# Optimization experiments

Measured on AMD Instinct MI355X. Metric: run time of the kernel, lower is better.

The kernel has to match this reference:

```python
import jax, jax.numpy as jnp
import numpy as np
import math

B, L, H, NH = 8, 200, 128, 2
HD = H // NH  # head dim = 64
TIME_VOCAB = 32
LN_EPS = 1e-12


def setup_inputs() -> dict:
    key = jax.random.key(0)
    ks = jax.random.split(key, 16)
    rn = lambda k, shape, s=0.02: (jax.random.normal(k, shape, jnp.float32) * s)
    return {
        "input_tensor": jax.random.normal(ks[0], (B, L, H), jnp.float32),
        "time_seq": jnp.sort(jax.random.randint(ks[1], (B, L), 0, 100000, jnp.int64), axis=-1),
        "attention_mask": jnp.zeros((B, 1, L, L), jnp.float32),
        "Wq": rn(ks[2], (H, H)), "bq": jnp.zeros((H,), jnp.float32),
        "Wk": rn(ks[3], (H, H)), "bk": jnp.zeros((H,), jnp.float32),
        "Wv": rn(ks[4], (H, H)), "bv": jnp.zeros((H,), jnp.float32),
        "Wd": rn(ks[5], (H, H)), "bd": jnp.zeros((H,), jnp.float32),
        "ln_g": jnp.ones((H,), jnp.float32), "ln_b": jnp.zeros((H,), jnp.float32),
        "key_time_table": rn(ks[6], (TIME_VOCAB, H)),
        "value_time_table": rn(ks[7], (TIME_VOCAB, H)),
        "key_pos_table": rn(ks[8], (L, H)),
        "value_pos_table": rn(ks[9], (L, H)),
    }


def _split_heads(x):
    # [B, L, H] -> [B, NH, L, HD]
    b, l, _ = x.shape
    return x.reshape(b, l, NH, HD).transpose(0, 2, 1, 3)


def reference(input_tensor, time_seq, attention_mask,
              Wq, bq, Wk, bk, Wv, bv, Wd, bd, ln_g, ln_b,
              key_time_table, value_time_table, key_pos_table, value_pos_table):
    b, l, h = input_tensor.shape

    # position embeddings (same for all batches)
    kpos = key_pos_table[:l].reshape(l, NH, HD).transpose(1, 0, 2)[None]    # [1,NH,L,HD]
    vpos = value_pos_table[:l].reshape(l, NH, HD).transpose(1, 0, 2)[None]  # [1,NH,L,HD]

    q = _split_heads(input_tensor @ Wq + bq)  # [B,NH,L,HD]
    k = _split_heads(input_tensor @ Wk + bk)
    v = _split_heads(input_tensor @ Wv + bv)

    scores = jnp.einsum('bhqd,bhkd->bhqk', q, k + kpos)

    # time decay: diff[b,i,j] = floor(log(1 + |t_i - t_j|))
    t = time_seq
    diff_idx = jnp.log1p(jnp.abs(t[:, :, None] - t[:, None, :]).astype(jnp.float32)).astype(jnp.int32)  # [B,L,L]

    # [B,L,L,H] -> [B,NH,L,L,HD]
    kt = key_time_table[diff_idx].reshape(b, l, l, NH, HD).transpose(0, 3, 1, 2, 4)
    vt = value_time_table[diff_idx].reshape(b, l, l, NH, HD).transpose(0, 3, 1, 2, 4)

    time_scores = jnp.einsum('bhqd,bhqkd->bhqk', q, kt)

    scores = (scores + time_scores) / math.sqrt(HD)
    scores = scores + attention_mask  # additive mask, broadcast over heads

    probs = jax.nn.softmax(scores, axis=-1)  # attn_dropout is identity in eval

    ctx = jnp.einsum('bhqk,bhkd->bhqd', probs, v + vpos)
    # NOTE: original uses raw (masked, pre-softmax) attention_scores here
    time_ctx = jnp.einsum('bhqk,bhqkd->bhqd', scores, vt)
    ctx = ctx + time_ctx

    ctx = ctx.transpose(0, 2, 1, 3).reshape(b, l, h)  # merge heads
    hidden = ctx @ Wd + bd                            # out_dropout identity in eval

    x = hidden + input_tensor
    mu = x.mean(-1, keepdims=True)
    var = ((x - mu) ** 2).mean(-1, keepdims=True)
    return (x - mu) / jnp.sqrt(var + LN_EPS) * ln_g + ln_b
```

## Files before the change

kernel.cpp:

```cpp
#include <hip/hip_runtime.h>
#include <math.h>

#define B_ 8
#define L_ 200
#define H_ 128
#define NH_ 2
#define HD_ 64
#define LP_ 256
#define TV_ 32

__global__ void zero_kt_kernel(float* __restrict__ kt){
    kt[blockIdx.x * 256 + threadIdx.x] = 0.f;
}

__global__ __launch_bounds__(128)
void qkv_kernel(const float* __restrict__ X,
                const float* __restrict__ Wq, const float* __restrict__ bq,
                const float* __restrict__ Wk, const float* __restrict__ bk,
                const float* __restrict__ Wv, const float* __restrict__ bv,
                const float* __restrict__ kpt, const float* __restrict__ vpt,
                float* __restrict__ Q, float* __restrict__ Kt, float* __restrict__ Vp){
    const int row = blockIdx.x;
    const int m   = blockIdx.y;
    const int j   = threadIdx.x;
    const int b   = row / L_, l = row % L_;
    __shared__ float xs[H_];
    xs[j] = X[row * H_ + j];
    __syncthreads();
    const float* W = (m == 0) ? Wq : ((m == 1) ? Wk : Wv);
    float acc = 0.f;
    #pragma unroll 8
    for (int i = 0; i < H_; ++i) acc += xs[i] * W[i * H_ + j];
    const int h = j >> 6, d = j & 63;
    if (m == 0) {
        Q[row * H_ + j] = acc + bq[j];
    } else if (m == 1) {
        float v = acc + bk[j] + kpt[l * H_ + j];
        Kt[(((b * NH_ + h) * HD_) + d) * LP_ + l] = v;
    } else {
        float v = acc + bv[j] + vpt[l * H_ + j];
        Vp[(((b * NH_ + h) * L_) + l) * HD_ + d] = v;
    }
}

__global__ __launch_bounds__(256)
void attn_kernel(const float* __restrict__ Q, const float* __restrict__ Kt,
                 const float* __restrict__ Vp, const int* __restrict__ tseq,
                 const float* __restrict__ mask,
                 const float* __restrict__ ktt, const float* __restrict__ vtt,
                 float* __restrict__ ctx){
    const int wave = threadIdx.x >> 6, lane = threadIdx.x & 63;
    const int gq = blockIdx.x * 4 + wave;
    const int q  = gq % L_;
    const int bh = gq / L_;
    const int h  = bh % NH_, b = bh / NH_;

    __shared__ __align__(16) float qs [4][HD_];
    __shared__            float qkt[4][TV_];
    __shared__            float ss [4][TV_];
    __shared__ __align__(16) float ps [4][LP_];

    qs[wave][lane] = Q[(b * L_ + q) * H_ + h * HD_ + lane];
    if (lane < TV_) ss[wave][lane] = 0.f;
    __syncthreads();

    if (lane < TV_) {
        float a = 0.f;
        #pragma unroll 8
        for (int d = 0; d < HD_; ++d) a += qs[wave][d] * ktt[lane * H_ + h * HD_ + d];
        qkt[wave][lane] = a;
    }
    __syncthreads();

    const int tq = tseq[b * L_ + q];

    const float4* kt4 = (const float4*)(Kt + (size_t)bh * HD_ * LP_);
    float4 s4 = make_float4(0.f, 0.f, 0.f, 0.f);
    #pragma unroll 4
    for (int d = 0; d < HD_; ++d) {
        const float qd = qs[wave][d];
        const float4 kv = kt4[d * (LP_ / 4) + lane];
        s4.x += qd * kv.x; s4.y += qd * kv.y; s4.z += qd * kv.z; s4.w += qd * kv.w;
    }
    float sv[4] = {s4.x, s4.y, s4.z, s4.w};
    const int k0 = lane * 4;
    float mx = -INFINITY;
    #pragma unroll
    for (int jj = 0; jj < 4; ++jj) {
        const int k = k0 + jj;
        if (k < L_) {
            int dt = tq - tseq[b * L_ + k]; if (dt < 0) dt = -dt;
            int idx = (int)log1pf((float)dt);
            if (idx > TV_ - 1) idx = TV_ - 1;
            float s = (sv[jj] + qkt[wave][idx]) * 0.125f
                      + mask[((size_t)b * L_ + q) * L_ + k];
            sv[jj] = s;
            atomicAdd(&ss[wave][idx], s);
            if (s > mx) mx = s;
        } else sv[jj] = -INFINITY;
    }
    for (int off = 32; off; off >>= 1) { float o = __shfl_xor(mx, off); if (o > mx) mx = o; }
    float sum = 0.f, ev[4];
    #pragma unroll
    for (int jj = 0; jj < 4; ++jj) {
        float e = (k0 + jj < L_) ? __expf(sv[jj] - mx) : 0.f;
        ev[jj] = e; sum += e;
    }
    for (int off = 32; off; off >>= 1) sum += __shfl_xor(sum, off);
    ((float4*)ps[wave])[lane] = make_float4(ev[0], ev[1], ev[2], ev[3]);
    __syncthreads();

    const float inv = 1.f / sum;
    const float* vp = Vp + (size_t)bh * L_ * HD_;
    float c = 0.f;
    #pragma unroll 4
    for (int k = 0; k < L_; ++k) c += ps[wave][k] * vp[k * HD_ + lane];
    c *= inv;
    float tc = 0.f;
    #pragma unroll 8
    for (int i = 0; i < TV_; ++i) tc += ss[wave][i] * vtt[i * H_ + h * HD_ + lane];
    ctx[((size_t)b * L_ + q) * H_ + h * HD_ + lane] = c + tc;
}

__global__ __launch_bounds__(128)
void out_kernel(const float* __restrict__ ctx, const float* __restrict__ Wd,
                const float* __restrict__ bd, const float* __restrict__ X,
                const float* __restrict__ g, const float* __restrict__ bb,
                float* __restrict__ out){
    const int row = blockIdx.x, j = threadIdx.x;
    __shared__ float cs[H_];
    __shared__ float red[4];
    cs[j] = ctx[row * H_ + j];
    __syncthreads();
    float acc = 0.f;
    #pragma unroll 8
    for (int i = 0; i < H_; ++i) acc += cs[i] * Wd[i * H_ + j];
    const float x = acc + bd[j] + X[row * H_ + j];

    const int wave = j >> 6, lane = j & 63;
    float s = x;
    for (int off = 32; off; off >>= 1) s += __shfl_xor(s, off);
    if (lane == 0) red[wave] = s;
    __syncthreads();
    const float mean = (red[0] + red[1]) * (1.f / H_);
    const float dx = x - mean;
    float s2 = dx * dx;
    for (int off = 32; off; off >>= 1) s2 += __shfl_xor(s2, off);
    if (lane == 0) red[wave + 2] = s2;
    __syncthreads();
    const float var = (red[2] + red[3]) * (1.f / H_);
    const float y = dx * rsqrtf(var + 1e-12f) * g[j] + bb[j];
    out[row * H_ + j] = y;
}

extern "C" void kernel_launch(void* const* d_in, const int* in_sizes, int n_in,
                              void* d_out, int out_size, void* d_ws, size_t ws_size,
                              hipStream_t stream) {
    const float* X    = (const float*)d_in[0];
    const int*   tseq = (const int*)  d_in[1];
    const float* mask = (const float*)d_in[2];
    const float* Wq = (const float*)d_in[3],  *bq = (const float*)d_in[4];
    const float* Wk = (const float*)d_in[5],  *bk = (const float*)d_in[6];
    const float* Wv = (const float*)d_in[7],  *bv = (const float*)d_in[8];
    const float* Wd = (const float*)d_in[9],  *bd = (const float*)d_in[10];
    const float* g  = (const float*)d_in[11], *bb = (const float*)d_in[12];
    const float* ktt = (const float*)d_in[13], *vtt = (const float*)d_in[14];
    const float* kpt = (const float*)d_in[15], *vpt = (const float*)d_in[16];

    float* ws  = (float*)d_ws;
    float* Q   = ws;
    float* Kt  = Q   + B_ * L_ * H_;
    float* Vp  = Kt  + B_ * NH_ * HD_ * LP_;
    float* ctx = Vp  + B_ * L_ * H_;

    zero_kt_kernel<<<B_ * NH_ * HD_ * LP_ / 256, 256, 0, stream>>>(Kt);
    dim3 g1(B_ * L_, 3);
    qkv_kernel<<<g1, 128, 0, stream>>>(X, Wq, bq, Wk, bk, Wv, bv, kpt, vpt, Q, Kt, Vp);
    attn_kernel<<<B_ * NH_ * L_ / 4, 256, 0, stream>>>(Q, Kt, Vp, tseq, mask, ktt, vtt, ctx);
    out_kernel<<<B_ * L_, 128, 0, stream>>>(ctx, Wd, bd, X, g, bb, (float*)d_out);
}
```

Before: 141.5 us.

## Fuse attention with output projection and LayerNorm, batch QKV rows per block

Merges the attention kernel and the output-projection/LayerNorm kernel into one 512-thread kernel per batch and 4 queries, keeping ctx in shared memory instead of a global round trip. The QKV projection now computes 8 rows per block so each weight load is reused across rows. The Kt zeroing kernel is removed, and mask and time_seq reads are vectorised. Several __syncthreads are dropped on the basis that each wave only touches its own shared slices. Padded Kt columns are no longer zeroed and can hold stale data, but their scores are forced to -inf.

```diff
diff --git a/kernel.cpp b/kernel.cpp
--- a/kernel.cpp
+++ b/kernel.cpp
@@ -8,10 +8,8 @@
 #define HD_ 64
 #define LP_ 256
 #define TV_ 32
-
-__global__ void zero_kt_kernel(float* __restrict__ kt){
-    kt[blockIdx.x * 256 + threadIdx.x] = 0.f;
-}
+#define RQ_ 8
+#define TQ_ 4
 
 __global__ __launch_bounds__(128)
 void qkv_kernel(const float* __restrict__ X,
@@ -20,84 +18,104 @@
                 const float* __restrict__ Wv, const float* __restrict__ bv,
                 const float* __restrict__ kpt, const float* __restrict__ vpt,
                 float* __restrict__ Q, float* __restrict__ Kt, float* __restrict__ Vp){
-    const int row = blockIdx.x;
-    const int m   = blockIdx.y;
-    const int j   = threadIdx.x;
-    const int b   = row / L_, l = row % L_;
-    __shared__ float xs[H_];
-    xs[j] = X[row * H_ + j];
+    const int r0 = blockIdx.x * RQ_;
+    const int m  = blockIdx.y;
+    const int j  = threadIdx.x;
+    __shared__ float xs[RQ_][H_];
+    #pragma unroll
+    for (int r = 0; r < RQ_; ++r) xs[r][j] = X[(r0 + r) * H_ + j];
     __syncthreads();
     const float* W = (m == 0) ? Wq : ((m == 1) ? Wk : Wv);
-    float acc = 0.f;
-    #pragma unroll 8
-    for (int i = 0; i < H_; ++i) acc += xs[i] * W[i * H_ + j];
+    float acc[RQ_];
+    #pragma unroll
+    for (int r = 0; r < RQ_; ++r) acc[r] = 0.f;
+    #pragma unroll 4
+    for (int i = 0; i < H_; ++i) {
+        const float w = W[i * H_ + j];
+        #pragma unroll
+        for (int r = 0; r < RQ_; ++r) acc[r] += xs[r][i] * w;
+    }
     const int h = j >> 6, d = j & 63;
     if (m == 0) {
-        Q[row * H_ + j] = acc + bq[j];
+        const float bj = bq[j];
+        #pragma unroll
+        for (int r = 0; r < RQ_; ++r) Q[(r0 + r) * H_ + j] = acc[r] + bj;
     } else if (m == 1) {
-        float v = acc + bk[j] + kpt[l * H_ + j];
-        Kt[(((b * NH_ + h) * HD_) + d) * LP_ + l] = v;
+        const float bj = bk[j];
+        #pragma unroll
+        for (int r = 0; r < RQ_; ++r) {
+            const int row = r0 + r, b = row / L_, l = row % L_;
+            Kt[((b * NH_ + h) * HD_ + d) * LP_ + l] = acc[r] + bj + kpt[l * H_ + j];
+        }
     } else {
-        float v = acc + bv[j] + vpt[l * H_ + j];
-        Vp[(((b * NH_ + h) * L_) + l) * HD_ + d] = v;
+        const float bj = bv[j];
+        #pragma unroll
+        for (int r = 0; r < RQ_; ++r) {
+            const int row = r0 + r, b = row / L_, l = row % L_;
+            Vp[((b * NH_ + h) * L_ + l) * HD_ + d] = acc[r] + bj + vpt[l * H_ + j];
+        }
     }
 }
 
-__global__ __launch_bounds__(256)
-void attn_kernel(const float* __restrict__ Q, const float* __restrict__ Kt,
-                 const float* __restrict__ Vp, const int* __restrict__ tseq,
-                 const float* __restrict__ mask,
-                 const float* __restrict__ ktt, const float* __restrict__ vtt,
-                 float* __restrict__ ctx){
-    const int wave = threadIdx.x >> 6, lane = threadIdx.x & 63;
-    const int gq = blockIdx.x * 4 + wave;
-    const int q  = gq % L_;
-    const int bh = gq / L_;
-    const int h  = bh % NH_, b = bh / NH_;
+__global__ __launch_bounds__(512)
+void attn_out_kernel(const float* __restrict__ Q, const float* __restrict__ Kt,
+                     const float* __restrict__ Vp, const int* __restrict__ tseq,
+                     const float* __restrict__ mask,
+                     const float* __restrict__ ktt, const float* __restrict__ vtt,
+                     const float* __restrict__ Wd, const float* __restrict__ bd,
+                     const float* __restrict__ X, const float* __restrict__ g,
+                     const float* __restrict__ bb, float* __restrict__ out){
+    const int b  = blockIdx.x / (L_ / TQ_);
+    const int q0 = (blockIdx.x % (L_ / TQ_)) * TQ_;
+    const int w  = threadIdx.x >> 6, lane = threadIdx.x & 63;
+    const int h  = w & 1, qr = w >> 1, q = q0 + qr;
+    const int bh = b * NH_ + h;
 
-    __shared__ __align__(16) float qs [4][HD_];
-    __shared__            float qkt[4][TV_];
-    __shared__            float ss [4][TV_];
-    __shared__ __align__(16) float ps [4][LP_];
+    __shared__ __align__(16) float qs [8][HD_];
+    __shared__ float qkt[8][TV_];
+    __shared__ float ss [8][TV_];
+    __shared__ __align__(16) float ps [8][LP_];
+    __shared__ float ctx_s[TQ_][H_];
+    __shared__ float red1[8], red2[8];
 
-    qs[wave][lane] = Q[(b * L_ + q) * H_ + h * HD_ + lane];
-    if (lane < TV_) ss[wave][lane] = 0.f;
-    __syncthreads();
-
+    qs[w][lane] = Q[(b * L_ + q) * H_ + h * HD_ + lane];
+    if (lane < TV_) ss[w][lane] = 0.f;
     if (lane < TV_) {
         float a = 0.f;
         #pragma unroll 8
-        for (int d = 0; d < HD_; ++d) a += qs[wave][d] * ktt[lane * H_ + h * HD_ + d];
-        qkt[wave][lane] = a;
+        for (int d = 0; d < HD_; ++d) a += qs[w][d] * ktt[lane * H_ + h * HD_ + d];
+        qkt[w][lane] = a;
     }
-    __syncthreads();
-
-    const int tq = tseq[b * L_ + q];
 
     const float4* kt4 = (const float4*)(Kt + (size_t)bh * HD_ * LP_);
     float4 s4 = make_float4(0.f, 0.f, 0.f, 0.f);
     #pragma unroll 4
     for (int d = 0; d < HD_; ++d) {
-        const float qd = qs[wave][d];
+        const float qd = qs[w][d];
         const float4 kv = kt4[d * (LP_ / 4) + lane];
         s4.x += qd * kv.x; s4.y += qd * kv.y; s4.z += qd * kv.z; s4.w += qd * kv.w;
     }
     float sv[4] = {s4.x, s4.y, s4.z, s4.w};
     const int k0 = lane * 4;
     float mx = -INFINITY;
-    #pragma unroll
-    for (int jj = 0; jj < 4; ++jj) {
-        const int k = k0 + jj;
-        if (k < L_) {
-            int dt = tq - tseq[b * L_ + k]; if (dt < 0) dt = -dt;
+    if (k0 < L_) {
+        const float4 m4 = ((const float4*)(mask + ((size_t)(b * L_ + q)) * L_))[lane];
+        const int4   t4 = ((const int4*)(tseq + b * L_))[lane];
+        const int    tq = tseq[b * L_ + q];
+        const float mv[4] = {m4.x, m4.y, m4.z, m4.w};
+        const int   tk[4] = {t4.x, t4.y, t4.z, t4.w};
+        #pragma unroll
+        for (int jj = 0; jj < 4; ++jj) {
+            int dt = tq - tk[jj]; if (dt < 0) dt = -dt;
             int idx = (int)log1pf((float)dt);
             if (idx > TV_ - 1) idx = TV_ - 1;
-            float s = (sv[jj] + qkt[wave][idx]) * 0.125f
-                      + mask[((size_t)b * L_ + q) * L_ + k];
+            float s = (sv[jj] + qkt[w][idx]) * 0.125f + mv[jj];
             sv[jj] = s;
-            atomicAdd(&ss[wave][idx], s);
+            atomicAdd(&ss[w][idx], s);
             if (s > mx) mx = s;
-        } else sv[jj] = -INFINITY;
+        }
+    } else {
+        sv[0] = sv[1] = sv[2] = sv[3] = -INFINITY;
     }
     for (int off = 32; off; off >>= 1) { float o = __shfl_xor(mx, off); if (o > mx) mx = o; }
     float sum = 0.f, ev[4];
@@ -107,48 +125,38 @@
         ev[jj] = e; sum += e;
     }
     for (int off = 32; off; off >>= 1) sum += __shfl_xor(sum, off);
-    ((float4*)ps[wave])[lane] = make_float4(ev[0], ev[1], ev[2], ev[3]);
-    __syncthreads();
+    ((float4*)ps[w])[lane] = make_float4(ev[0], ev[1], ev[2], ev[3]);
 
     const float inv = 1.f / sum;
     const float* vp = Vp + (size_t)bh * L_ * HD_;
     float c = 0.f;
     #pragma unroll 4
-    for (int k = 0; k < L_; ++k) c += ps[wave][k] * vp[k * HD_ + lane];
+    for (int k = 0; k < L_; ++k) c += ps[w][k] * vp[k * HD_ + lane];
     c *= inv;
     float tc = 0.f;
     #pragma unroll 8
-    for (int i = 0; i < TV_; ++i) tc += ss[wave][i] * vtt[i * H_ + h * HD_ + lane];
-    ctx[((size_t)b * L_ + q) * H_ + h * HD_ + lane] = c + tc;
-}
+    for (int i = 0; i < TV_; ++i) tc += ss[w][i] * vtt[i * H_ + h * HD_ + lane];
+    ctx_s[qr][h * HD_ + lane] = c + tc;
+    __syncthreads();
 
-__global__ __launch_bounds__(128)
-void out_kernel(const float* __restrict__ ctx, const float* __restrict__ Wd,
-                const float* __restrict__ bd, const float* __restrict__ X,
-                const float* __restrict__ g, const float* __restrict__ bb,
-                float* __restrict__ out){
-    const int row = blockIdx.x, j = threadIdx.x;
-    __shared__ float cs[H_];
-    __shared__ float red[4];
-    cs[j] = ctx[row * H_ + j];
-    __syncthreads();
+    const int r = threadIdx.x >> 7, j = threadIdx.x & 127;
     float acc = 0.f;
     #pragma unroll 8
-    for (int i = 0; i < H_; ++i) acc += cs[i] * Wd[i * H_ + j];
+    for (int i = 0; i < H_; ++i) acc += ctx_s[r][i] * Wd[i * H_ + j];
+    const int row = b * L_ + q0 + r;
     const float x = acc + bd[j] + X[row * H_ + j];
 
-    const int wave = j >> 6, lane = j & 63;
     float s = x;
     for (int off = 32; off; off >>= 1) s += __shfl_xor(s, off);
-    if (lane == 0) red[wave] = s;
+    if (lane == 0) red1[w] = s;
     __syncthreads();
-    const float mean = (red[0] + red[1]) * (1.f / H_);
+    const float mean = (red1[2 * r] + red1[2 * r + 1]) * (1.f / H_);
     const float dx = x - mean;
     float s2 = dx * dx;
     for (int off = 32; off; off >>= 1) s2 += __shfl_xor(s2, off);
-    if (lane == 0) red[wave + 2] = s2;
+    if (lane == 0) red2[w] = s2;
     __syncthreads();
-    const float var = (red[2] + red[3]) * (1.f / H_);
+    const float var = (red2[2 * r] + red2[2 * r + 1]) * (1.f / H_);
     const float y = dx * rsqrtf(var + 1e-12f) * g[j] + bb[j];
     out[row * H_ + j] = y;
 }
@@ -171,11 +179,9 @@
     float* Q   = ws;
     float* Kt  = Q   + B_ * L_ * H_;
     float* Vp  = Kt  + B_ * NH_ * HD_ * LP_;
-    float* ctx = Vp  + B_ * L_ * H_;
 
-    zero_kt_kernel<<<B_ * NH_ * HD_ * LP_ / 256, 256, 0, stream>>>(Kt);
-    dim3 g1(B_ * L_, 3);
+    dim3 g1(B_ * L_ / RQ_, 3);
     qkv_kernel<<<g1, 128, 0, stream>>>(X, Wq, bq, Wk, bk, Wv, bv, kpt, vpt, Q, Kt, Vp);
-    attn_kernel<<<B_ * NH_ * L_ / 4, 256, 0, stream>>>(Q, Kt, Vp, tseq, mask, ktt, vtt, ctx);
-    out_kernel<<<B_ * L_, 128, 0, stream>>>(ctx, Wd, bd, X, g, bb, (float*)d_out);
+    attn_out_kernel<<<B_ * (L_ / TQ_), 512, 0, stream>>>(Q, Kt, Vp, tseq, mask, ktt, vtt,
+                                                         Wd, bd, X, g, bb, (float*)d_out);
 }
```

Measured after the change: 140.7 us. No clear change (-0.6%).
